# Performance work log

Measured on AMD Instinct MI355X. Metric: run time of the kernel, lower is better.

Reference implementation:

```python
import jax, jax.numpy as jnp
import numpy as np

N, C, HD = 8192, 1024, 128

def setup_inputs() -> dict:
    key = jax.random.key(0)
    ks = jax.random.split(key, 9)
    def xavier(k, fan_in, fan_out):
        lim = float(np.sqrt(6.0 / (fan_in + fan_out)))
        return jax.random.uniform(k, (fan_out, fan_in), jnp.float32, -lim, lim)
    return {
        "x": jax.random.normal(ks[0], (N, C), jnp.float32),
        "Wq": xavier(ks[1], C, HD), "bq": jnp.zeros((HD,), jnp.float32),
        "Wk": xavier(ks[2], C, HD), "bk": jnp.zeros((HD,), jnp.float32),
        "Wv": xavier(ks[3], C, C),  "bv": jnp.zeros((C,), jnp.float32),
        "Wo": xavier(ks[4], C, C),  "bo": jnp.zeros((C,), jnp.float32),
    }

def reference(x, Wq, bq, Wk, bk, Wv, bv, Wo, bo):
    scale = HD ** -0.5
    q = x @ Wq.T + bq          # (N, HD)
    k = x @ Wk.T + bk          # (N, HD)
    v = x @ Wv.T + bv          # (N, C)
    scores = (q @ k.T) * scale # (N, N)
    attn = jax.nn.softmax(scores, axis=-1)
    out = attn @ v             # (N, C)
    return out @ Wo.T + bo
```

## Files before the change

kernel.cpp:

```cpp
#include <hip/hip_runtime.h>

#define NTOK 8192
#define CDIM 1024
#define HDIM 128

typedef __attribute__((ext_vector_type(8))) short short8;
typedef __attribute__((ext_vector_type(4))) float floatx4;
typedef __attribute__((ext_vector_type(4))) unsigned short ushort4v;

__device__ inline unsigned short f2bf(float f) {
    union { float f; unsigned u; } v; v.f = f;
    unsigned r = v.u + 0x7fffu + ((v.u >> 16) & 1u);
    return (unsigned short)(r >> 16);
}
__device__ inline unsigned short f2bf_fast(float f) {
    union { float f; unsigned u; } v; v.f = f;
    return (unsigned short)((v.u + 0x8000u) >> 16);
}
__device__ inline float bf2f(short s) {
    union { unsigned u; float f; } v;
    v.u = ((unsigned)(unsigned short)s) << 16;
    return v.f;
}
__device__ inline void async16(const unsigned short* g, short* l) {
    __builtin_amdgcn_global_load_lds(
        (const __attribute__((address_space(1))) unsigned*)g,
        (__attribute__((address_space(3))) unsigned*)l, 16, 0, 0);
}

__global__ void cast_f32_bf16(const float* __restrict__ in,
                              unsigned short* __restrict__ out, int n4) {
    int i = blockIdx.x * blockDim.x + threadIdx.x;
    if (i < n4) {
        float4 v = ((const float4*)in)[i];
        ushort4 o;
        o.x = f2bf(v.x); o.y = f2bf(v.y); o.z = f2bf(v.z); o.w = f2bf(v.w);
        ((ushort4*)out)[i] = o;
    }
}

template<int SWZ>
__global__ __launch_bounds__(256) void gemm_nt(
    const unsigned short* __restrict__ A, const unsigned short* __restrict__ W,
    const float* __restrict__ bias, unsigned short* __restrict__ out, int M, int N, int K)
{
    __shared__ short As[4][64][8];
    __shared__ short Ws[4][64][8];
    const int tid = threadIdx.x;
    const int wave = tid >> 6, lane = tid & 63;
    const int lr = lane & 15, lc = lane >> 4;
    const int m0 = blockIdx.x * 64, n0 = blockIdx.y * 64;

    floatx4 acc[4] = {};
    const int srow = tid >> 2, sch = tid & 3;
    const unsigned short* Ag = A + (long)(m0 + srow) * K + sch * 8;
    const unsigned short* Wg = W + (long)(n0 + srow) * K + sch * 8;

    for (int k0 = 0; k0 < K; k0 += 32) {
        *(short8*)&As[sch][srow][0] = *(const short8*)(Ag + k0);
        *(short8*)&Ws[sch][srow][0] = *(const short8*)(Wg + k0);
        __syncthreads();
        short8 a = *(short8*)&As[lc][wave * 16 + lr][0];
#pragma unroll
        for (int s = 0; s < 4; s++) {
            short8 b = *(short8*)&Ws[lc][s * 16 + lr][0];
            acc[s] = __builtin_amdgcn_mfma_f32_16x16x32_bf16(a, b, acc[s], 0, 0, 0);
        }
        __syncthreads();
    }

#pragma unroll
    for (int s = 0; s < 4; s++) {
        int h = n0 + s * 16 + lr;
        float bv = bias[h];
        int tok0 = m0 + wave * 16 + lc * 4;
#pragma unroll
        for (int r = 0; r < 4; r++) {
            int tok = tok0 + r;
            if (SWZ)
                out[(tok >> 5) * 4096 + (h >> 3) * 256 + (tok & 31) * 8 + (h & 7)] =
                    f2bf(acc[s][r] + bv);
            else
                out[(long)tok * N + h] = f2bf(acc[s][r] + bv);
        }
    }
}

template<int MODE>
__global__ __launch_bounds__(256) void gemm128_nt(
    const unsigned short* __restrict__ A, const unsigned short* __restrict__ W,
    const float* __restrict__ bias, void* __restrict__ out, int M, int N, int K)
{
    __shared__ short As[128][4][8];
    __shared__ short Ws[128][4][8];
    const int tid = threadIdx.x, wave = tid >> 6, lane = tid & 63;
    const int lr = lane & 15, lc = lane >> 4;
    const int wm = (wave >> 1) * 64, wn = (wave & 1) * 64;
    const int m0 = blockIdx.x * 128, n0 = blockIdx.y * 128;

    floatx4 acc[4][4] = {};

    const int srow = lane >> 2, sch = lane & 3;
    const unsigned short* Ag0 = A + (long)(m0 + wave * 32 + srow) * K + sch * 8;
    const unsigned short* Ag1 = Ag0 + (long)16 * K;
    const unsigned short* Wg0 = W + (long)(n0 + wave * 32 + srow) * K + sch * 8;
    const unsigned short* Wg1 = Wg0 + (long)16 * K;
    short* lA0 = &As[wave * 32][0][0];
    short* lA1 = &As[wave * 32 + 16][0][0];
    short* lW0 = &Ws[wave * 32][0][0];
    short* lW1 = &Ws[wave * 32 + 16][0][0];

    for (int k0 = 0; k0 < K; k0 += 32) {
        async16(Ag0 + k0, lA0);
        async16(Ag1 + k0, lA1);
        async16(Wg0 + k0, lW0);
        async16(Wg1 + k0, lW1);
        __syncthreads();
        short8 af[4], bfg[4];
#pragma unroll
        for (int i = 0; i < 4; i++) af[i]  = *(short8*)&As[wm + i * 16 + lr][lc][0];
#pragma unroll
        for (int j = 0; j < 4; j++) bfg[j] = *(short8*)&Ws[wn + j * 16 + lr][lc][0];
#pragma unroll
        for (int i = 0; i < 4; i++)
#pragma unroll
            for (int j = 0; j < 4; j++)
                acc[i][j] = __builtin_amdgcn_mfma_f32_16x16x32_bf16(af[i], bfg[j], acc[i][j], 0, 0, 0);
        __syncthreads();
    }

#pragma unroll
    for (int i = 0; i < 4; i++) {
        int t0 = m0 + wm + i * 16 + lc * 4;
#pragma unroll
        for (int j = 0; j < 4; j++) {
            int c = n0 + wn + j * 16 + lr;
            float bv = bias[c];
            if (MODE == 0) {
                float* o = (float*)out;
#pragma unroll
                for (int r = 0; r < 4; r++) o[(long)(t0 + r) * N + c] = acc[i][j][r] + bv;
            } else {
                unsigned short* o = (unsigned short*)out;
                ushort4 pk;
                pk.x = f2bf(acc[i][j][0] + bv); pk.y = f2bf(acc[i][j][1] + bv);
                pk.z = f2bf(acc[i][j][2] + bv); pk.w = f2bf(acc[i][j][3] + bv);
                long off = (long)(c >> 8) * 2097152 + (t0 >> 5) * 8192 +
                           ((t0 & 31) >> 3) * 2048 + (c & 255) * 8 + (t0 & 7);
                *(ushort4*)&o[off] = pk;
            }
        }
    }
}

__global__ __launch_bounds__(512, 2) void attn_pv(
    const unsigned short* __restrict__ qb, const unsigned short* __restrict__ ksw,
    const unsigned short* __restrict__ vsw,
    unsigned short* __restrict__ Oa, unsigned short* __restrict__ Ob,
    float* __restrict__ la, float* __restrict__ lb)
{
    __shared__ short Ks[2][2][16][32][8];
    __shared__ short Vs[2][2][4][256][8];
    __shared__ short Ps[8][32][40];

    const int tid = threadIdx.x, wave = tid >> 6, lane = tid & 63;
    const int lr = lane & 15, lc = lane >> 4;
    const int m0 = blockIdx.x * 256, cblk = blockIdx.y;
    const int mw = m0 + wave * 32;
    const int nt0 = blockIdx.z * 128;
    unsigned short* Op = blockIdx.z ? Ob : Oa;
    float* ls = blockIdx.z ? lb : la;
    const float cexp = (float)(0.08838834764831845 * 1.4426950408889634);

    short8 qf[2][4];
#pragma unroll
    for (int ms = 0; ms < 2; ms++)
#pragma unroll
        for (int kk = 0; kk < 4; kk++)
            qf[ms][kk] = *(const short8*)&qb[(mw + ms * 16 + lr) * HDIM + kk * 32 + lc * 8];

    floatx4 acc[2][16] = {};
    float lsum[2] = {};

    const unsigned short* kg = ksw + wave * 512 + lane * 8;
    short* const klb = &Ks[0][0][0][0][0];
    const unsigned short* vg[2];
    short* const vlb = &Vs[0][0][0][0][0];
#pragma unroll
    for (int t = 0; t < 2; t++)
        vg[t] = vsw + (long)cblk * 2097152 + (wave * 2 + t) * 512 + lane * 8;

#pragma unroll
    for (int h = 0; h < 2; h++) {
        long nt = nt0 + h;
        async16(kg + nt * 4096, klb + h * 4096 + wave * 512);
#pragma unroll
        for (int t = 0; t < 2; t++)
            async16(vg[t] + nt * 8192, vlb + h * 8192 + (wave * 2 + t) * 512);
    }

    for (int it = 0; it < 64; ++it) {
        const int buf = it & 1;
        __syncthreads();
        if (it + 1 < 64) {
#pragma unroll
            for (int h = 0; h < 2; h++) {
                long nt = nt0 + 2 * (it + 1) + h;
                async16(kg + nt * 4096,
                        klb + (buf ^ 1) * 8192 + h * 4096 + wave * 512);
#pragma unroll
                for (int t = 0; t < 2; t++)
                    async16(vg[t] + nt * 8192,
                            vlb + (buf ^ 1) * 16384 + h * 8192 + (wave * 2 + t) * 512);
            }
        }

#pragma unroll
        for (int h = 0; h < 2; h++) {
            floatx4 st[2][2] = {};
#pragma unroll
            for (int kk = 0; kk < 4; kk++) {
                short8 kf0 = *(short8*)&Ks[buf][h][kk * 4 + lc][lr][0];
                short8 kf1 = *(short8*)&Ks[buf][h][kk * 4 + lc][16 + lr][0];
#pragma unroll
                for (int ms = 0; ms < 2; ms++) {
                    st[ms][0] = __builtin_amdgcn_mfma_f32_16x16x32_bf16(kf0, qf[ms][kk], st[ms][0], 0, 0, 0);
                    st[ms][1] = __builtin_amdgcn_mfma_f32_16x16x32_bf16(kf1, qf[ms][kk], st[ms][1], 0, 0, 0);
                }
            }
#pragma unroll
            for (int ms = 0; ms < 2; ms++)
#pragma unroll
                for (int sub = 0; sub < 2; sub++) {
                    ushort4v pk;
#pragma unroll
                    for (int r = 0; r < 4; r++) {
                        float p = __builtin_amdgcn_exp2f(st[ms][sub][r] * cexp);
                        lsum[ms] += p;
                        pk[r] = f2bf_fast(p);
                    }
                    *(ushort4v*)&Ps[wave][ms * 16 + lr][sub * 16 + lc * 4] = pk;
                }
            short8 ap[2];
#pragma unroll
            for (int ms = 0; ms < 2; ms++) ap[ms] = *(short8*)&Ps[wave][ms * 16 + lr][lc * 8];
#pragma unroll
            for (int csh = 0; csh < 2; csh++) {
                short8 bv[8];
#pragma unroll
                for (int cs = 0; cs < 8; cs++)
                    bv[cs] = *(short8*)&Vs[buf][h][lc][(csh * 8 + cs) * 16 + lr][0];
#pragma unroll
                for (int ms = 0; ms < 2; ms++)
#pragma unroll
                    for (int cs = 0; cs < 8; cs++)
                        acc[ms][csh * 8 + cs] =
                            __builtin_amdgcn_mfma_f32_16x16x32_bf16(ap[ms], bv[cs], acc[ms][csh * 8 + cs], 0, 0, 0);
            }
        }
    }

#pragma unroll
    for (int ms = 0; ms < 2; ms++)
#pragma unroll
        for (int cs = 0; cs < 16; cs++) {
            int c = cblk * 256 + cs * 16 + lr;
#pragma unroll
            for (int r = 0; r < 4; r++)
                Op[(long)(mw + ms * 16 + lc * 4 + r) * CDIM + c] = f2bf(acc[ms][cs][r]);
        }
    if (blockIdx.y == 0) {
#pragma unroll
        for (int ms = 0; ms < 2; ms++) {
            lsum[ms] += __shfl_xor(lsum[ms], 16);
            lsum[ms] += __shfl_xor(lsum[ms], 32);
        }
        if (lc == 0) {
#pragma unroll
            for (int ms = 0; ms < 2; ms++) ls[mw + ms * 16 + lr] = lsum[ms];
        }
    }
}

__global__ __launch_bounds__(256) void combine_attn(
    const unsigned short* __restrict__ Oa, unsigned short* __restrict__ Ob,
    const float* __restrict__ la, const float* __restrict__ lb)
{
    int i = blockIdx.x * blockDim.x + threadIdx.x;
    int row = i >> 7;
    float inv = 1.0f / (la[row] + lb[row]);
    short8 a = ((const short8*)Oa)[i];
    short8 b = ((const short8*)Ob)[i];
    short8 o;
#pragma unroll
    for (int e = 0; e < 8; e++) o[e] = (short)f2bf((bf2f(a[e]) + bf2f(b[e])) * inv);
    ((short8*)Ob)[i] = o;
}

extern "C" void kernel_launch(void* const* d_in, const int* in_sizes, int n_in,
                              void* d_out, int out_size, void* d_ws, size_t ws_size,
                              hipStream_t stream) {
    const float* x  = (const float*)d_in[0];
    const float* Wq = (const float*)d_in[1];
    const float* bq = (const float*)d_in[2];
    const float* Wk = (const float*)d_in[3];
    const float* bk = (const float*)d_in[4];
    const float* Wv = (const float*)d_in[5];
    const float* bv = (const float*)d_in[6];
    const float* Wo = (const float*)d_in[7];
    const float* bo = (const float*)d_in[8];

    char* ws = (char*)d_ws;
    unsigned short* x_bf   = (unsigned short*)(ws + 0);
    unsigned short* wq_bf  = (unsigned short*)(ws + 16777216);
    unsigned short* wk_bf  = (unsigned short*)(ws + 17039360);
    unsigned short* wv_bf  = (unsigned short*)(ws + 17301504);
    unsigned short* wo_bf  = (unsigned short*)(ws + 19398656);
    unsigned short* q_bf   = (unsigned short*)(ws + 21495808);
    unsigned short* k_swz  = (unsigned short*)(ws + 23592960);
    unsigned short* v_swz  = (unsigned short*)(ws + 25690112);
    unsigned short* attn_bf= (unsigned short*)(ws + 42467328);
    float* lsum_a          = (float*)(ws + 59244544);
    float* lsum_b          = (float*)(ws + 59277312);

    cast_f32_bf16<<<8192, 256, 0, stream>>>(x,  x_bf,  2097152);
    cast_f32_bf16<<<128,  256, 0, stream>>>(Wq, wq_bf, 32768);
    cast_f32_bf16<<<128,  256, 0, stream>>>(Wk, wk_bf, 32768);
    cast_f32_bf16<<<1024, 256, 0, stream>>>(Wv, wv_bf, 262144);
    cast_f32_bf16<<<1024, 256, 0, stream>>>(Wo, wo_bf, 262144);

    gemm_nt<0><<<dim3(128, 2), 256, 0, stream>>>(x_bf, wq_bf, bq, q_bf, NTOK, HDIM, CDIM);
    gemm_nt<1><<<dim3(128, 2), 256, 0, stream>>>(x_bf, wk_bf, bk, k_swz, NTOK, HDIM, CDIM);
    gemm128_nt<2><<<dim3(64, 8), 256, 0, stream>>>(x_bf, wv_bf, bv, v_swz, NTOK, CDIM, CDIM);

    attn_pv<<<dim3(32, 4, 2), 512, 0, stream>>>(q_bf, k_swz, v_swz,
                                                x_bf, attn_bf, lsum_a, lsum_b);
    combine_attn<<<4096, 256, 0, stream>>>(x_bf, attn_bf, lsum_a, lsum_b);

    gemm128_nt<0><<<dim3(64, 8), 256, 0, stream>>>(attn_bf, wo_bf, bo, d_out, NTOK, CDIM, CDIM);
}
```

Baseline: 391.7 us.

## Halve attention row tile per wave and key stage to double block count

The attention kernel now gives each wave 16 query rows instead of 32 and stages one 32-key tile per iteration instead of two, doubling the grid along rows and halving shared memory. Launch bounds now ask for 4 blocks per CU, which increases parallelism and occupancy (the old grid of 256 blocks underfilled the GPU). In exchange, each K/V tile loaded into LDS is reused by half as many rows, which doubles total K/V traffic and the number of barriers.

```diff
diff --git a/kernel.cpp b/kernel.cpp
--- a/kernel.cpp
+++ b/kernel.cpp
@@ -153,132 +153,105 @@
     }
 }
 
-__global__ __launch_bounds__(512, 2) void attn_pv(
+__global__ __launch_bounds__(512, 4) void attn_pv(
     const unsigned short* __restrict__ qb, const unsigned short* __restrict__ ksw,
     const unsigned short* __restrict__ vsw,
     unsigned short* __restrict__ Oa, unsigned short* __restrict__ Ob,
     float* __restrict__ la, float* __restrict__ lb)
 {
-    __shared__ short Ks[2][2][16][32][8];
-    __shared__ short Vs[2][2][4][256][8];
-    __shared__ short Ps[8][32][40];
+    __shared__ short Ks[2][16][32][8];
+    __shared__ short Vs[2][4][256][8];
+    __shared__ short Ps[8][16][40];
 
     const int tid = threadIdx.x, wave = tid >> 6, lane = tid & 63;
     const int lr = lane & 15, lc = lane >> 4;
-    const int m0 = blockIdx.x * 256, cblk = blockIdx.y;
-    const int mw = m0 + wave * 32;
+    const int m0 = blockIdx.x * 128, cblk = blockIdx.y;
+    const int mw = m0 + wave * 16;
     const int nt0 = blockIdx.z * 128;
     unsigned short* Op = blockIdx.z ? Ob : Oa;
     float* ls = blockIdx.z ? lb : la;
     const float cexp = (float)(0.08838834764831845 * 1.4426950408889634);
 
-    short8 qf[2][4];
-#pragma unroll
-    for (int ms = 0; ms < 2; ms++)
-#pragma unroll
-        for (int kk = 0; kk < 4; kk++)
-            qf[ms][kk] = *(const short8*)&qb[(mw + ms * 16 + lr) * HDIM + kk * 32 + lc * 8];
-
-    floatx4 acc[2][16] = {};
-    float lsum[2] = {};
+    short8 qf[4];
+#pragma unroll
+    for (int kk = 0; kk < 4; kk++)
+        qf[kk] = *(const short8*)&qb[(mw + lr) * HDIM + kk * 32 + lc * 8];
+
+    floatx4 acc[16] = {};
+    float lsum = 0.f;
 
     const unsigned short* kg = ksw + wave * 512 + lane * 8;
-    short* const klb = &Ks[0][0][0][0][0];
+    short* const klb = &Ks[0][0][0][0];
     const unsigned short* vg[2];
-    short* const vlb = &Vs[0][0][0][0][0];
+    short* const vlb = &Vs[0][0][0][0];
 #pragma unroll
     for (int t = 0; t < 2; t++)
         vg[t] = vsw + (long)cblk * 2097152 + (wave * 2 + t) * 512 + lane * 8;
 
-#pragma unroll
-    for (int h = 0; h < 2; h++) {
-        long nt = nt0 + h;
-        async16(kg + nt * 4096, klb + h * 4096 + wave * 512);
+    {
+        long nt = nt0;
+        async16(kg + nt * 4096, klb + wave * 512);
 #pragma unroll
         for (int t = 0; t < 2; t++)
-            async16(vg[t] + nt * 8192, vlb + h * 8192 + (wave * 2 + t) * 512);
-    }
-
-    for (int it = 0; it < 64; ++it) {
+            async16(vg[t] + nt * 8192, vlb + (wave * 2 + t) * 512);
+    }
+
+    for (int it = 0; it < 128; ++it) {
         const int buf = it & 1;
         __syncthreads();
-        if (it + 1 < 64) {
-#pragma unroll
-            for (int h = 0; h < 2; h++) {
-                long nt = nt0 + 2 * (it + 1) + h;
-                async16(kg + nt * 4096,
-                        klb + (buf ^ 1) * 8192 + h * 4096 + wave * 512);
-#pragma unroll
-                for (int t = 0; t < 2; t++)
-                    async16(vg[t] + nt * 8192,
-                            vlb + (buf ^ 1) * 16384 + h * 8192 + (wave * 2 + t) * 512);
+        if (it + 1 < 128) {
+            long nt = nt0 + it + 1;
+            async16(kg + nt * 4096, klb + (buf ^ 1) * 4096 + wave * 512);
+#pragma unroll
+            for (int t = 0; t < 2; t++)
+                async16(vg[t] + nt * 8192,
+                        vlb + (buf ^ 1) * 8192 + (wave * 2 + t) * 512);
+        }
+
+        floatx4 st[2] = {};
+#pragma unroll
+        for (int kk = 0; kk < 4; kk++) {
+            short8 kf0 = *(short8*)&Ks[buf][kk * 4 + lc][lr][0];
+            short8 kf1 = *(short8*)&Ks[buf][kk * 4 + lc][16 + lr][0];
+            st[0] = __builtin_amdgcn_mfma_f32_16x16x32_bf16(kf0, qf[kk], st[0], 0, 0, 0);
+            st[1] = __builtin_amdgcn_mfma_f32_16x16x32_bf16(kf1, qf[kk], st[1], 0, 0, 0);
+        }
+#pragma unroll
+        for (int sub = 0; sub < 2; sub++) {
+            ushort4v pk;
+#pragma unroll
+            for (int r = 0; r < 4; r++) {
+                float p = __builtin_amdgcn_exp2f(st[sub][r] * cexp);
+                lsum += p;
+                pk[r] = f2bf_fast(p);
             }
-        }
-
-#pragma unroll
-        for (int h = 0; h < 2; h++) {
-            floatx4 st[2][2] = {};
-#pragma unroll
-            for (int kk = 0; kk < 4; kk++) {
-                short8 kf0 = *(short8*)&Ks[buf][h][kk * 4 + lc][lr][0];
-                short8 kf1 = *(short8*)&Ks[buf][h][kk * 4 + lc][16 + lr][0];
-#pragma unroll
-                for (int ms = 0; ms < 2; ms++) {
-                    st[ms][0] = __builtin_amdgcn_mfma_f32_16x16x32_bf16(kf0, qf[ms][kk], st[ms][0], 0, 0, 0);
-                    st[ms][1] = __builtin_amdgcn_mfma_f32_16x16x32_bf16(kf1, qf[ms][kk], st[ms][1], 0, 0, 0);
-                }
-            }
-#pragma unroll
-            for (int ms = 0; ms < 2; ms++)
-#pragma unroll
-                for (int sub = 0; sub < 2; sub++) {
-                    ushort4v pk;
-#pragma unroll
-                    for (int r = 0; r < 4; r++) {
-                        float p = __builtin_amdgcn_exp2f(st[ms][sub][r] * cexp);
-                        lsum[ms] += p;
-                        pk[r] = f2bf_fast(p);
-                    }
-                    *(ushort4v*)&Ps[wave][ms * 16 + lr][sub * 16 + lc * 4] = pk;
-                }
-            short8 ap[2];
-#pragma unroll
-            for (int ms = 0; ms < 2; ms++) ap[ms] = *(short8*)&Ps[wave][ms * 16 + lr][lc * 8];
-#pragma unroll
-            for (int csh = 0; csh < 2; csh++) {
-                short8 bv[8];
-#pragma unroll
-                for (int cs = 0; cs < 8; cs++)
-                    bv[cs] = *(short8*)&Vs[buf][h][lc][(csh * 8 + cs) * 16 + lr][0];
-#pragma unroll
-                for (int ms = 0; ms < 2; ms++)
-#pragma unroll
-                    for (int cs = 0; cs < 8; cs++)
-                        acc[ms][csh * 8 + cs] =
-                            __builtin_amdgcn_mfma_f32_16x16x32_bf16(ap[ms], bv[cs], acc[ms][csh * 8 + cs], 0, 0, 0);
-            }
-        }
-    }
-
-#pragma unroll
-    for (int ms = 0; ms < 2; ms++)
-#pragma unroll
-        for (int cs = 0; cs < 16; cs++) {
-            int c = cblk * 256 + cs * 16 + lr;
-#pragma unroll
-            for (int r = 0; r < 4; r++)
-                Op[(long)(mw + ms * 16 + lc * 4 + r) * CDIM + c] = f2bf(acc[ms][cs][r]);
-        }
+            *(ushort4v*)&Ps[wave][lr][sub * 16 + lc * 4] = pk;
+        }
+        short8 ap = *(short8*)&Ps[wave][lr][lc * 8];
+#pragma unroll
+        for (int csh = 0; csh < 2; csh++) {
+            short8 bv[8];
+#pragma unroll
+            for (int cs = 0; cs < 8; cs++)
+                bv[cs] = *(short8*)&Vs[buf][lc][(csh * 8 + cs) * 16 + lr][0];
+#pragma unroll
+            for (int cs = 0; cs < 8; cs++)
+                acc[csh * 8 + cs] =
+                    __builtin_amdgcn_mfma_f32_16x16x32_bf16(ap, bv[cs], acc[csh * 8 + cs], 0, 0, 0);
+        }
+    }
+
+#pragma unroll
+    for (int cs = 0; cs < 16; cs++) {
+        int c = cblk * 256 + cs * 16 + lr;
+#pragma unroll
+        for (int r = 0; r < 4; r++)
+            Op[(long)(mw + lc * 4 + r) * CDIM + c] = f2bf(acc[cs][r]);
+    }
     if (blockIdx.y == 0) {
-#pragma unroll
-        for (int ms = 0; ms < 2; ms++) {
-            lsum[ms] += __shfl_xor(lsum[ms], 16);
-            lsum[ms] += __shfl_xor(lsum[ms], 32);
-        }
-        if (lc == 0) {
-#pragma unroll
-            for (int ms = 0; ms < 2; ms++) ls[mw + ms * 16 + lr] = lsum[ms];
-        }
+        lsum += __shfl_xor(lsum, 16);
+        lsum += __shfl_xor(lsum, 32);
+        if (lc == 0) ls[mw + lr] = lsum;
     }
 }
 
@@ -333,7 +306,7 @@
     gemm_nt<1><<<dim3(128, 2), 256, 0, stream>>>(x_bf, wk_bf, bk, k_swz, NTOK, HDIM, CDIM);
     gemm128_nt<2><<<dim3(64, 8), 256, 0, stream>>>(x_bf, wv_bf, bv, v_swz, NTOK, CDIM, CDIM);
 
-    attn_pv<<<dim3(32, 4, 2), 512, 0, stream>>>(q_bf, k_swz, v_swz,
+    attn_pv<<<dim3(64, 4, 2), 512, 0, stream>>>(q_bf, k_swz, v_swz,
                                                 x_bf, attn_bf, lsum_a, lsum_b);
     combine_attn<<<4096, 256, 0, stream>>>(x_bf, attn_bf, lsum_a, lsum_b);
 
```

Measured after the change: 422.6 us. +7.9%, slower.

## Shrink attention blocks to 4 waves with single key tile per stage

Applied to the files above, without the earlier changes.

The attention kernel moves from 512-thread blocks covering 256 query rows to 256-thread blocks covering 128 rows, launching twice as many blocks. Each pipeline stage now loads one 32-key tile instead of two, halving shared memory for K and V and running 128 iterations instead of 64. The aim is more resident blocks and better latency hiding per CU. In exchange, each K/V tile is reused by half as many query rows, which doubles K/V traffic, and barriers per key are doubled.

```diff
diff --git a/kernel.cpp b/kernel.cpp
--- a/kernel.cpp
+++ b/kernel.cpp
@@ -153,19 +153,19 @@
     }
 }
 
-__global__ __launch_bounds__(512, 2) void attn_pv(
+__global__ __launch_bounds__(256, 2) void attn_pv(
     const unsigned short* __restrict__ qb, const unsigned short* __restrict__ ksw,
     const unsigned short* __restrict__ vsw,
     unsigned short* __restrict__ Oa, unsigned short* __restrict__ Ob,
     float* __restrict__ la, float* __restrict__ lb)
 {
-    __shared__ short Ks[2][2][16][32][8];
-    __shared__ short Vs[2][2][4][256][8];
-    __shared__ short Ps[8][32][40];
+    __shared__ short Ks[2][16][32][8];
+    __shared__ short Vs[2][4][256][8];
+    __shared__ short Ps[4][32][40];
 
     const int tid = threadIdx.x, wave = tid >> 6, lane = tid & 63;
     const int lr = lane & 15, lc = lane >> 4;
-    const int m0 = blockIdx.x * 256, cblk = blockIdx.y;
+    const int m0 = blockIdx.x * 128, cblk = blockIdx.y;
     const int mw = m0 + wave * 32;
     const int nt0 = blockIdx.z * 128;
     unsigned short* Op = blockIdx.z ? Ob : Oa;
@@ -182,81 +182,79 @@
     floatx4 acc[2][16] = {};
     float lsum[2] = {};
 
-    const unsigned short* kg = ksw + wave * 512 + lane * 8;
-    short* const klb = &Ks[0][0][0][0][0];
-    const unsigned short* vg[2];
-    short* const vlb = &Vs[0][0][0][0][0];
-#pragma unroll
-    for (int t = 0; t < 2; t++)
-        vg[t] = vsw + (long)cblk * 2097152 + (wave * 2 + t) * 512 + lane * 8;
-
-#pragma unroll
-    for (int h = 0; h < 2; h++) {
-        long nt = nt0 + h;
-        async16(kg + nt * 4096, klb + h * 4096 + wave * 512);
+    const unsigned short* kg[2];
+    short* const klb = &Ks[0][0][0][0];
+#pragma unroll
+    for (int t = 0; t < 2; t++) kg[t] = ksw + (wave * 2 + t) * 512 + lane * 8;
+    const unsigned short* vg[4];
+    short* const vlb = &Vs[0][0][0][0];
+#pragma unroll
+    for (int t = 0; t < 4; t++)
+        vg[t] = vsw + (long)cblk * 2097152 + (wave * 4 + t) * 512 + lane * 8;
+
+    {
+        long nt = nt0;
 #pragma unroll
         for (int t = 0; t < 2; t++)
-            async16(vg[t] + nt * 8192, vlb + h * 8192 + (wave * 2 + t) * 512);
-    }
-
-    for (int it = 0; it < 64; ++it) {
+            async16(kg[t] + nt * 4096, klb + (wave * 2 + t) * 512);
+#pragma unroll
+        for (int t = 0; t < 4; t++)
+            async16(vg[t] + nt * 8192, vlb + (wave * 4 + t) * 512);
+    }
+
+    for (int it = 0; it < 128; ++it) {
         const int buf = it & 1;
         __syncthreads();
-        if (it + 1 < 64) {
-#pragma unroll
-            for (int h = 0; h < 2; h++) {
-                long nt = nt0 + 2 * (it + 1) + h;
-                async16(kg + nt * 4096,
-                        klb + (buf ^ 1) * 8192 + h * 4096 + wave * 512);
-#pragma unroll
-                for (int t = 0; t < 2; t++)
-                    async16(vg[t] + nt * 8192,
-                            vlb + (buf ^ 1) * 16384 + h * 8192 + (wave * 2 + t) * 512);
+        if (it + 1 < 128) {
+            long nt = nt0 + it + 1;
+#pragma unroll
+            for (int t = 0; t < 2; t++)
+                async16(kg[t] + nt * 4096, klb + (buf ^ 1) * 4096 + (wave * 2 + t) * 512);
+#pragma unroll
+            for (int t = 0; t < 4; t++)
+                async16(vg[t] + nt * 8192,
+                        vlb + (buf ^ 1) * 8192 + (wave * 4 + t) * 512);
+        }
+
+        floatx4 st[2][2] = {};
+#pragma unroll
+        for (int kk = 0; kk < 4; kk++) {
+            short8 kf0 = *(short8*)&Ks[buf][kk * 4 + lc][lr][0];
+            short8 kf1 = *(short8*)&Ks[buf][kk * 4 + lc][16 + lr][0];
+#pragma unroll
+            for (int ms = 0; ms < 2; ms++) {
+                st[ms][0] = __builtin_amdgcn_mfma_f32_16x16x32_bf16(kf0, qf[ms][kk], st[ms][0], 0, 0, 0);
+                st[ms][1] = __builtin_amdgcn_mfma_f32_16x16x32_bf16(kf1, qf[ms][kk], st[ms][1], 0, 0, 0);
             }
         }
-
-#pragma unroll
-        for (int h = 0; h < 2; h++) {
-            floatx4 st[2][2] = {};
-#pragma unroll
-            for (int kk = 0; kk < 4; kk++) {
-                short8 kf0 = *(short8*)&Ks[buf][h][kk * 4 + lc][lr][0];
-                short8 kf1 = *(short8*)&Ks[buf][h][kk * 4 + lc][16 + lr][0];
-#pragma unroll
-                for (int ms = 0; ms < 2; ms++) {
-                    st[ms][0] = __builtin_amdgcn_mfma_f32_16x16x32_bf16(kf0, qf[ms][kk], st[ms][0], 0, 0, 0);
-                    st[ms][1] = __builtin_amdgcn_mfma_f32_16x16x32_bf16(kf1, qf[ms][kk], st[ms][1], 0, 0, 0);
+#pragma unroll
+        for (int ms = 0; ms < 2; ms++)
+#pragma unroll
+            for (int sub = 0; sub < 2; sub++) {
+                ushort4v pk;
+#pragma unroll
+                for (int r = 0; r < 4; r++) {
+                    float p = __builtin_amdgcn_exp2f(st[ms][sub][r] * cexp);
+                    lsum[ms] += p;
+                    pk[r] = f2bf_fast(p);
                 }
+                *(ushort4v*)&Ps[wave][ms * 16 + lr][sub * 16 + lc * 4] = pk;
             }
+        short8 ap[2];
+#pragma unroll
+        for (int ms = 0; ms < 2; ms++) ap[ms] = *(short8*)&Ps[wave][ms * 16 + lr][lc * 8];
+#pragma unroll
+        for (int csh = 0; csh < 2; csh++) {
+            short8 bv[8];
+#pragma unroll
+            for (int cs = 0; cs < 8; cs++)
+                bv[cs] = *(short8*)&Vs[buf][lc][(csh * 8 + cs) * 16 + lr][0];
 #pragma unroll
             for (int ms = 0; ms < 2; ms++)
 #pragma unroll
-                for (int sub = 0; sub < 2; sub++) {
-                    ushort4v pk;
-#pragma unroll
-                    for (int r = 0; r < 4; r++) {
-                        float p = __builtin_amdgcn_exp2f(st[ms][sub][r] * cexp);
-                        lsum[ms] += p;
-                        pk[r] = f2bf_fast(p);
-                    }
-                    *(ushort4v*)&Ps[wave][ms * 16 + lr][sub * 16 + lc * 4] = pk;
-                }
-            short8 ap[2];
-#pragma unroll
-            for (int ms = 0; ms < 2; ms++) ap[ms] = *(short8*)&Ps[wave][ms * 16 + lr][lc * 8];
-#pragma unroll
-            for (int csh = 0; csh < 2; csh++) {
-                short8 bv[8];
-#pragma unroll
                 for (int cs = 0; cs < 8; cs++)
-                    bv[cs] = *(short8*)&Vs[buf][h][lc][(csh * 8 + cs) * 16 + lr][0];
-#pragma unroll
-                for (int ms = 0; ms < 2; ms++)
-#pragma unroll
-                    for (int cs = 0; cs < 8; cs++)
-                        acc[ms][csh * 8 + cs] =
-                            __builtin_amdgcn_mfma_f32_16x16x32_bf16(ap[ms], bv[cs], acc[ms][csh * 8 + cs], 0, 0, 0);
-            }
+                    acc[ms][csh * 8 + cs] =
+                        __builtin_amdgcn_mfma_f32_16x16x32_bf16(ap[ms], bv[cs], acc[ms][csh * 8 + cs], 0, 0, 0);
         }
     }
 
@@ -333,7 +331,7 @@
     gemm_nt<1><<<dim3(128, 2), 256, 0, stream>>>(x_bf, wk_bf, bk, k_swz, NTOK, HDIM, CDIM);
     gemm128_nt<2><<<dim3(64, 8), 256, 0, stream>>>(x_bf, wv_bf, bv, v_swz, NTOK, CDIM, CDIM);
 
-    attn_pv<<<dim3(32, 4, 2), 512, 0, stream>>>(q_bf, k_swz, v_swz,
+    attn_pv<<<dim3(64, 4, 2), 256, 0, stream>>>(q_bf, k_swz, v_swz,
                                                 x_bf, attn_bf, lsum_a, lsum_b);
     combine_attn<<<4096, 256, 0, stream>>>(x_bf, attn_bf, lsum_a, lsum_b);
 
```

After: 400.7 us. 1.02x slower.
